# Kernel optimization log

Measured on AMD Instinct MI355X. Metric: run time of the kernel, lower is better.

## Reference

```python
import jax, jax.numpy as jnp
import numpy as np

EPS = 1e-5
TAU = 0.1

def _bn(x, g, b):
    # BatchNorm1d in training mode: batch statistics (biased variance)
    mu = jnp.mean(x, axis=0, keepdims=True)
    var = jnp.var(x, axis=0, keepdims=True)
    return (x - mu) * jax.lax.rsqrt(var + EPS) * g + b

def setup_inputs():
    key = jax.random.key(0)
    ks = jax.random.split(key, 8)
    B, D, H, L, P, C, ND, NP = 32768, 2048, 1024, 384, 192, 10, 2, 2
    s = 0.02
    u = jax.random.uniform(ks[7], (B, NP), minval=1e-6, maxval=1.0 - 1e-6)
    return {
        'x': jax.random.normal(ks[0], (B, D), dtype=jnp.float32),
        'W_pre': jax.random.normal(ks[1], (H, D), dtype=jnp.float32) * s,
        'b_pre': jnp.zeros((H,), jnp.float32),
        'g_pre': jnp.ones((H,), jnp.float32),
        'be_pre': jnp.zeros((H,), jnp.float32),
        'W_disc': jax.random.normal(ks[2], (L, H), dtype=jnp.float32) * s,
        'b_disc': jnp.zeros((L,), jnp.float32),
        'g_disc': jnp.ones((L,), jnp.float32),
        'be_disc': jnp.zeros((L,), jnp.float32),
        'W_dfc': jax.random.normal(ks[3], (ND, L), dtype=jnp.float32) * s,
        'b_dfc': jnp.zeros((ND,), jnp.float32),
        'W_sw': jax.random.normal(ks[4], (NP, L), dtype=jnp.float32) * s,
        'b_sw': jnp.zeros((NP,), jnp.float32),
        'W1': jax.random.normal(ks[5], (NP, P, H), dtype=jnp.float32) * s,
        'b1': jnp.zeros((NP, P), jnp.float32),
        'W2': jax.random.normal(ks[6], (NP, C, P), dtype=jnp.float32) * s,
        'b2': jnp.zeros((NP, C), jnp.float32),
        'gumbel_noise': -jnp.log(-jnp.log(u)),
    }

def reference(x, W_pre, b_pre, g_pre, be_pre, W_disc, b_disc, g_disc, be_disc,
              W_dfc, b_dfc, W_sw, b_sw, W1, b1, W2, b2, gumbel_noise):
    # pre_classifier: Linear + BN + ReLU
    feature = jax.nn.relu(_bn(x @ W_pre.T + b_pre, g_pre, be_pre))
    # GRL is identity in forward
    dp = jax.nn.relu(_bn(feature @ W_disc.T + b_disc, g_disc, be_disc))
    dom = dp @ W_dfc.T + b_dfc                      # [B, num_domains]
    sw = jax.nn.relu(dp @ W_sw.T + b_sw)            # [B, n_partition]
    gum = jax.nn.softmax((sw + gumbel_noise) / TAU, axis=-1)  # soft gumbel-softmax
    idx = jnp.argmax(gum, axis=-1)                  # [B] routing decision
    # compute both (tiny) experts densely, then select per sample (faithful math,
    # avoids per-sample gather of full weight matrices)
    h_all = jax.nn.relu(jnp.einsum('bd,epd->bep', feature, W1) + b1)  # [B,E,P]
    o_all = jnp.einsum('bep,ecp->bec', h_all, W2) + b2                # [B,E,C]
    out = jnp.take_along_axis(o_all, idx[:, None, None], axis=1)[:, 0]  # [B,C]
    # original: sum_p gum[b,p] * stacked (stacked has one entry) == out * sum(gum)
    cop = out * jnp.sum(gum, axis=-1, keepdims=True)
    return cop, dom, idx
```

## Files before the change

### kernel.cpp

```cpp
#include <hip/hip_runtime.h>
#include <math.h>

#define kB 32768
#define kD 2048
#define kH 1024
#define kL 384
#define kP 192
#define kC 10
#define kNP 2
#define kND 2
#define kNCAT 768
#define kTAU 0.1f
#define kEPS 1e-5f
#define NPART 256
#define SCALE 64.0f
#define INV_SC2 (1.0f / 4096.0f)

typedef _Float16 f16x8 __attribute__((ext_vector_type(8)));
typedef _Float16 f16x4 __attribute__((ext_vector_type(4)));
typedef float f32x16 __attribute__((ext_vector_type(16)));

__device__ __forceinline__ void gll16(const unsigned short* g, unsigned short* l)
{
    __builtin_amdgcn_global_load_lds(
        (const __attribute__((address_space(1))) unsigned int*)g,
        (__attribute__((address_space(3))) unsigned int*)l, 16, 0, 0);
}

__device__ __host__ __forceinline__ int key8(int r) { return (r ^ (r >> 3)) & 7; }

__global__ __launch_bounds__(256)
void split_pack(const float* __restrict__ in, unsigned short* __restrict__ out, int K)
{
    const int row = blockIdx.x;
    const int t = threadIdx.x;
    const int s = key8(row);
    const float* ir = in + (size_t)row * K;
    unsigned short* orow = out + (size_t)row * (K * 2);
    for (int k0 = t * 4; k0 < K; k0 += 1024) {
        const float4 v = *(const float4*)&ir[k0];
        const float a0 = v.x * SCALE, a1 = v.y * SCALE, a2 = v.z * SCALE, a3 = v.w * SCALE;
        const _Float16 h0 = (_Float16)a0, h1 = (_Float16)a1, h2 = (_Float16)a2, h3 = (_Float16)a3;
        const _Float16 l0 = (_Float16)(a0 - (float)h0), l1 = (_Float16)(a1 - (float)h1);
        const _Float16 l2 = (_Float16)(a2 - (float)h2), l3 = (_Float16)(a3 - (float)h3);
        const f16x4 hi = {h0, h1, h2, h3};
        const f16x4 lo = {l0, l1, l2, l3};
        const int kb = k0 >> 5, kk = k0 & 31;
        const int c = kk >> 3, off = kk & 7;
        *(f16x4*)&orow[kb * 64 + ((c ^ s) << 3) + off]       = hi;
        *(f16x4*)&orow[kb * 64 + (((c ^ 4) ^ s) << 3) + off] = lo;
    }
}

template<int KDIM, bool BN>
__global__ __launch_bounds__(512, 1)
void gemm_fused(const float* __restrict__ Afp,
                const unsigned short* __restrict__ Bpk,
                const float* __restrict__ bnsc, const float* __restrict__ bnsh,
                float* __restrict__ C, const int N, const int gridX,
                float* __restrict__ psum, float* __restrict__ psumsq, const int statN)
{
    constexpr int NKB = KDIM / 32;
    __shared__ unsigned short lds[4][256 * 64];

    const int t = threadIdx.x;
    const int lane = t & 63;
    const int w = t >> 6;
    const int wr = w >> 2, wc = w & 3;
    const int l31 = lane & 31, kg = lane >> 5;

    const int nwg = gridDim.x;
    const int chunk = nwg >> 3;
    const int bid = blockIdx.x;
    const int logical = (bid & 7) * chunk + (bid >> 3);
    const int bx = logical % gridX, by = logical / gridX;
    const int m0 = by * 256, n0 = bx * 256;

    const int arow = t >> 1;
    const int akh = t & 1;
    const int skey = key8(arow);
    const int c0 = akh * 2, c1 = akh * 2 + 1;
    const float* aSrc = Afp + (size_t)(m0 + arow) * KDIM + akh * 16;

    const size_t bstride = (size_t)NKB * 64;
    const unsigned short* bG[4];
    int bLoff[4];
#pragma unroll
    for (int it = 0; it < 4; ++it) {
        const int Q = (w * 4 + it) * 64 + lane;
        bG[it] = Bpk + (size_t)(n0 + (Q >> 3)) * bstride + (Q & 7) * 8;
        bLoff[it] = (w * 4 + it) * 512;
    }

    int keyA[4], keyB[2];
#pragma unroll
    for (int mi = 0; mi < 4; ++mi)
        keyA[mi] = (l31 & 7) ^ ((mi * 4 + (l31 >> 3)) & 7);
#pragma unroll
    for (int ni = 0; ni < 2; ++ni)
        keyB[ni] = (l31 & 7) ^ ((wc * 8 + ni * 4 + (l31 >> 3)) & 7);

    f32x16 acc[4][2];
#pragma unroll
    for (int mi = 0; mi < 4; ++mi)
#pragma unroll
        for (int ni = 0; ni < 2; ++ni)
#pragma unroll
            for (int r = 0; r < 16; ++r) acc[mi][ni][r] = 0.f;

    float4 av[4], scv[4], shv[4];

    auto stage_issue = [&](int kb, int buf) {
        const int kt = kb * 32;
#pragma unroll
        for (int it = 0; it < 4; ++it)
            gll16(bG[it] + (size_t)kb * 64, &lds[2 + buf][bLoff[it]]);
#pragma unroll
        for (int j = 0; j < 4; ++j)
            av[j] = *(const float4*)&aSrc[kt + j * 4];
        if constexpr (BN) {
#pragma unroll
            for (int j = 0; j < 4; ++j) {
                scv[j] = *(const float4*)&bnsc[kt + akh * 16 + j * 4];
                shv[j] = *(const float4*)&bnsh[kt + akh * 16 + j * 4];
            }
        }
    };

    auto stage_write = [&](int buf) {
        float v[16];
#pragma unroll
        for (int j = 0; j < 4; ++j) {
            float4 a = av[j];
            if constexpr (BN) {
                a.x = fmaxf(fmaf(a.x, scv[j].x, shv[j].x), 0.f);
                a.y = fmaxf(fmaf(a.y, scv[j].y, shv[j].y), 0.f);
                a.z = fmaxf(fmaf(a.z, scv[j].z, shv[j].z), 0.f);
                a.w = fmaxf(fmaf(a.w, scv[j].w, shv[j].w), 0.f);
            } else {
                a.x *= SCALE; a.y *= SCALE; a.z *= SCALE; a.w *= SCALE;
            }
            v[j * 4 + 0] = a.x; v[j * 4 + 1] = a.y;
            v[j * 4 + 2] = a.z; v[j * 4 + 3] = a.w;
        }
        f16x8 hi[2], lo[2];
#pragma unroll
        for (int h = 0; h < 2; ++h)
#pragma unroll
            for (int i = 0; i < 8; ++i) {
                const float x = v[h * 8 + i];
                const _Float16 hh = (_Float16)x;
                hi[h][i] = hh;
                lo[h][i] = (_Float16)(x - (float)hh);
            }
        unsigned short* dst = &lds[buf][arow * 64];
        *(f16x8*)&dst[(c0 ^ skey) * 8]       = hi[0];
        *(f16x8*)&dst[(c1 ^ skey) * 8]       = hi[1];
        *(f16x8*)&dst[((c0 ^ 4) ^ skey) * 8] = lo[0];
        *(f16x8*)&dst[((c1 ^ 4) ^ skey) * 8] = lo[1];
    };

    stage_issue(0, 0);
    stage_write(0);
    asm volatile("s_waitcnt vmcnt(0) lgkmcnt(0)" ::: "memory");
    __builtin_amdgcn_s_barrier();

    for (int kb = 0; kb < NKB; ++kb) {
        const int cur = kb & 1, nxt = cur ^ 1;
        const bool pf = (kb + 1 < NKB);
        if (pf) stage_issue(kb + 1, nxt);

        f16x8 bh[2][2], bl[2][2];
#pragma unroll
        for (int ni = 0; ni < 2; ++ni) {
            const unsigned short* bb = &lds[2 + cur][(wc * 64 + ni * 32 + l31) * 64];
#pragma unroll
            for (int ks = 0; ks < 2; ++ks) {
                const int lg = ks * 2 + kg;
                bh[ni][ks] = *(const f16x8*)&bb[((lg ^ keyB[ni]) << 3)];
                bl[ni][ks] = *(const f16x8*)&bb[(((lg ^ 4) ^ keyB[ni]) << 3)];
            }
        }
#pragma unroll
        for (int mi = 0; mi < 4; ++mi) {
            const unsigned short* ab = &lds[cur][(wr * 128 + mi * 32 + l31) * 64];
            f16x8 ah[2], al[2];
#pragma unroll
            for (int ks = 0; ks < 2; ++ks) {
                const int lg = ks * 2 + kg;
                ah[ks] = *(const f16x8*)&ab[((lg ^ keyA[mi]) << 3)];
                al[ks] = *(const f16x8*)&ab[(((lg ^ 4) ^ keyA[mi]) << 3)];
            }
#pragma unroll
            for (int ni = 0; ni < 2; ++ni)
#pragma unroll
                for (int ks = 0; ks < 2; ++ks) {
                    acc[mi][ni] = __builtin_amdgcn_mfma_f32_32x32x16_f16(ah[ks], bh[ni][ks], acc[mi][ni], 0, 0, 0);
                    acc[mi][ni] = __builtin_amdgcn_mfma_f32_32x32x16_f16(ah[ks], bl[ni][ks], acc[mi][ni], 0, 0, 0);
                    acc[mi][ni] = __builtin_amdgcn_mfma_f32_32x32x16_f16(al[ks], bh[ni][ks], acc[mi][ni], 0, 0, 0);
                }
        }
        if (pf) stage_write(nxt);
        asm volatile("s_waitcnt vmcnt(0) lgkmcnt(0)" ::: "memory");
        __builtin_amdgcn_s_barrier();
    }

#pragma unroll
    for (int mi = 0; mi < 4; ++mi)
#pragma unroll
        for (int ni = 0; ni < 2; ++ni) {
            const int colg = n0 + wc * 64 + ni * 32 + l31;
#pragma unroll
            for (int r = 0; r < 16; ++r) {
                const int row = m0 + wr * 128 + mi * 32 + (r & 3) + 8 * (r >> 2) + 4 * kg;
                C[(size_t)row * N + colg] = acc[mi][ni][r];
            }
        }

#pragma unroll
    for (int ni = 0; ni < 2; ++ni) {
        float s = 0.f, sq = 0.f;
#pragma unroll
        for (int mi = 0; mi < 4; ++mi)
#pragma unroll
            for (int r = 0; r < 16; ++r) {
                const float v = acc[mi][ni][r];
                s += v;
                sq = fmaf(v, v, sq);
            }
        s  += __shfl_xor(s, 32);
        sq += __shfl_xor(sq, 32);
        const int col = n0 + wc * 64 + ni * 32 + l31;
        if (lane < 32 && col < statN) {
            psum[(size_t)(by * 2 + wr) * statN + col]   = s;
            psumsq[(size_t)(by * 2 + wr) * statN + col] = sq;
        }
    }
}

__global__ __launch_bounds__(256)
void colstat_finalize(const float* __restrict__ psum, const float* __restrict__ psumsq,
                      int ncols, const float* __restrict__ g, const float* __restrict__ be,
                      float* __restrict__ scale, float* __restrict__ shift,
                      float inv_sc, float outsc)
{
    const int c = blockIdx.x * 256 + threadIdx.x;
    if (c >= ncols) return;
    float s = 0.f, sq = 0.f;
    for (int i = 0; i < NPART; ++i) {
        s  += psum[(size_t)i * ncols + c];
        sq += psumsq[(size_t)i * ncols + c];
    }
    const float mup = s * (1.f / kB);
    const float var = (sq * (1.f / kB) - mup * mup) * inv_sc * inv_sc;
    const float scl = outsc * g[c] * rsqrtf(var + kEPS) * inv_sc;
    scale[c] = scl;
    shift[c] = fmaf(-mup, scl, outsc * be[c]);
}

__global__ __launch_bounds__(256)
void tail_kernel(const float* __restrict__ Z2,
                 const float* __restrict__ scale2, const float* __restrict__ shift2,
                 const float* __restrict__ W_dfc, const float* __restrict__ b_dfc,
                 const float* __restrict__ W_sw, const float* __restrict__ b_sw,
                 const float* __restrict__ b1, const float* __restrict__ W2,
                 const float* __restrict__ b2, const float* __restrict__ noise,
                 float* __restrict__ out)
{
    __shared__ float sWdfc[kND * kL];
    __shared__ float sWsw[kNP * kL];
    __shared__ float sW2[kNP * kC * kP];
    __shared__ float sb1[kNP * kP];
    __shared__ float sScale[kL];
    __shared__ float sShift[kL];
    const int t = threadIdx.x;
    for (int i = t; i < kND * kL; i += 256) sWdfc[i] = W_dfc[i];
    for (int i = t; i < kNP * kL; i += 256) sWsw[i] = W_sw[i];
    for (int i = t; i < kNP * kC * kP; i += 256) sW2[i] = W2[i];
    for (int i = t; i < kNP * kP; i += 256) sb1[i] = b1[i];
    for (int i = t; i < kL; i += 256) { sScale[i] = scale2[i]; sShift[i] = shift2[i]; }
    __syncthreads();

    const int lane = t & 63;
    const int b = blockIdx.x * 4 + (t >> 6);
    const float* z = Z2 + (size_t)b * kNCAT;

    float d0 = 0.f, d1 = 0.f, s0 = 0.f, s1 = 0.f;
#pragma unroll
    for (int j = 0; j < 6; ++j) {
        const int k = lane + j * 64;
        const float dp = fmaxf(fmaf(z[k], sScale[k], sShift[k]), 0.f);
        d0 = fmaf(dp, sWdfc[k],      d0);
        d1 = fmaf(dp, sWdfc[kL + k], d1);
        s0 = fmaf(dp, sWsw[k],       s0);
        s1 = fmaf(dp, sWsw[kL + k],  s1);
    }
#pragma unroll
    for (int off = 32; off; off >>= 1) {
        d0 += __shfl_xor(d0, off);
        d1 += __shfl_xor(d1, off);
        s0 += __shfl_xor(s0, off);
        s1 += __shfl_xor(s1, off);
    }
    d0 += b_dfc[0];
    d1 += b_dfc[1];

    const float sw0 = fmaxf(s0 + b_sw[0], 0.f);
    const float sw1 = fmaxf(s1 + b_sw[1], 0.f);
    const float l0 = (sw0 + noise[(size_t)b * 2 + 0]) * (1.f / kTAU);
    const float l1 = (sw1 + noise[(size_t)b * 2 + 1]) * (1.f / kTAU);
    const float mx = fmaxf(l0, l1);
    const float e0 = expf(l0 - mx), e1 = expf(l1 - mx);
    const float inv = 1.f / (e0 + e1);
    const float sgum = e0 * inv + e1 * inv;
    const int idx = (l1 > l0) ? 1 : 0;

    const float* zh = z + kL + idx * kP;
    const float h0 = fmaxf(fmaf(zh[lane],       INV_SC2, sb1[idx * kP + lane]),       0.f);
    const float h1 = fmaxf(fmaf(zh[lane + 64],  INV_SC2, sb1[idx * kP + lane + 64]),  0.f);
    const float h2 = fmaxf(fmaf(zh[lane + 128], INV_SC2, sb1[idx * kP + lane + 128]), 0.f);

    float* cop  = out;
    float* dom  = out + (size_t)kB * kC;
    float* idxo = dom + (size_t)kB * kND;

#pragma unroll
    for (int c = 0; c < kC; ++c) {
        const float* wv = &sW2[(idx * kC + c) * kP];
        float oc = h0 * wv[lane] + h1 * wv[lane + 64] + h2 * wv[lane + 128];
#pragma unroll
        for (int off = 32; off; off >>= 1) oc += __shfl_xor(oc, off);
        if (lane == c) cop[(size_t)b * kC + c] = (oc + b2[idx * kC + c]) * sgum;
    }
    if (lane == 0) {
        dom[(size_t)b * 2 + 0] = d0;
        dom[(size_t)b * 2 + 1] = d1;
        idxo[b] = (float)idx;
    }
}

extern "C" void kernel_launch(void* const* d_in, const int* in_sizes, int n_in,
                              void* d_out, int out_size, void* d_ws, size_t ws_size,
                              hipStream_t stream)
{
    const float* x       = (const float*)d_in[0];
    const float* W_pre   = (const float*)d_in[1];
    const float* g_pre   = (const float*)d_in[3];
    const float* be_pre  = (const float*)d_in[4];
    const float* W_disc  = (const float*)d_in[5];
    const float* g_disc  = (const float*)d_in[7];
    const float* be_disc = (const float*)d_in[8];
    const float* W_dfc   = (const float*)d_in[9];
    const float* b_dfc   = (const float*)d_in[10];
    const float* W_sw    = (const float*)d_in[11];
    const float* b_sw    = (const float*)d_in[12];
    const float* W1      = (const float*)d_in[13];
    const float* b1      = (const float*)d_in[14];
    const float* W2      = (const float*)d_in[15];
    const float* b2      = (const float*)d_in[16];
    const float* noise   = (const float*)d_in[17];

    char* wsb = (char*)d_ws;
    unsigned short* Wps = (unsigned short*)wsb;
    unsigned short* Ws2 = (unsigned short*)(wsb + (size_t)1024 * 4096 * 2);
    float* Z1 = (float*)(wsb + (size_t)1024 * 4096 * 2 + (size_t)768 * 2048 * 2);
    float* Z2 = Z1 + (size_t)kB * kH;
    float* psum1  = Z2 + (size_t)kB * kNCAT;
    float* psq1   = psum1 + (size_t)NPART * kH;
    float* psum2  = psq1 + (size_t)NPART * kH;
    float* psq2   = psum2 + (size_t)NPART * kL;
    float* scale1 = psq2 + (size_t)NPART * kL;
    float* shift1 = scale1 + kH;
    float* scale2 = shift1 + kH;
    float* shift2 = scale2 + kL;
    float* out    = (float*)d_out;

    split_pack<<<dim3(kH), 256, 0, stream>>>(W_pre, Wps, kD);
    split_pack<<<dim3(kL), 256, 0, stream>>>(W_disc, Ws2, kH);
    split_pack<<<dim3(kNP * kP), 256, 0, stream>>>(W1, Ws2 + (size_t)kL * (2 * kH), kH);
    gemm_fused<kD, false><<<dim3(4 * 128), 512, 0, stream>>>(
        x, Wps, nullptr, nullptr, Z1, kH, 4, psum1, psq1, kH);
    colstat_finalize<<<dim3(kH / 256), 256, 0, stream>>>(psum1, psq1, kH, g_pre, be_pre,
                                                         scale1, shift1, INV_SC2, SCALE);
    gemm_fused<kH, true><<<dim3(3 * 128), 512, 0, stream>>>(
        Z1, Ws2, scale1, shift1, Z2, kNCAT, 3, psum2, psq2, kL);
    colstat_finalize<<<dim3((kL + 255) / 256), 256, 0, stream>>>(psum2, psq2, kL, g_disc, be_disc,
                                                                 scale2, shift2, INV_SC2, 1.0f);
    tail_kernel<<<dim3(kB / 4), 256, 0, stream>>>(Z2, scale2, shift2, W_dfc, b_dfc,
                                                  W_sw, b_sw, b1, W2, b2, noise, out);
}
```

Baseline: 691.1 us.

## Pre-split activations to fp16 hi/lo and stream both GEMM operands via LDS DMA

Adds separate passes that convert x, and later the BN+ReLU-applied Z1, into swizzled fp16 hi/lo packed buffers. Both GEMMs then load A and B tiles with global_load_lds DMA into 128x128 tiles at 256 threads with occupancy 3, replacing the 256x256 double-buffered kernel that converted A in registers. The aim is to take conversion ALU work and register pressure out of the GEMM inner loop and to rely on more resident workgroups for latency hiding. In exchange it adds extra global traffic: the packed x buffer is twice the size of x in fp32 and has to be written and then read back, and the main loop is single-buffered with two barriers per k-step.

```diff
diff --git a/kernel.cpp b/kernel.cpp
--- a/kernel.cpp
+++ b/kernel.cpp
@@ -12,12 +12,11 @@
 #define kNCAT 768
 #define kTAU 0.1f
 #define kEPS 1e-5f
-#define NPART 256
+#define NPART 512
 #define SCALE 64.0f
 #define INV_SC2 (1.0f / 4096.0f)
 
 typedef _Float16 f16x8 __attribute__((ext_vector_type(8)));
-typedef _Float16 f16x4 __attribute__((ext_vector_type(4)));
 typedef float f32x16 __attribute__((ext_vector_type(16)));
 
 __device__ __forceinline__ void gll16(const unsigned short* g, unsigned short* l)
@@ -27,192 +26,165 @@
         (__attribute__((address_space(3))) unsigned int*)l, 16, 0, 0);
 }
 
-__device__ __host__ __forceinline__ int key8(int r) { return (r ^ (r >> 3)) & 7; }
+__device__ __host__ __forceinline__ int wkey(int r)
+{
+    return (r & 1) | ((r & 2) << 1) | ((r & 4) >> 1);
+}
 
 __global__ __launch_bounds__(256)
-void split_pack(const float* __restrict__ in, unsigned short* __restrict__ out, int K)
-{
-    const int row = blockIdx.x;
-    const int t = threadIdx.x;
-    const int s = key8(row);
-    const float* ir = in + (size_t)row * K;
-    unsigned short* orow = out + (size_t)row * (K * 2);
-    for (int k0 = t * 4; k0 < K; k0 += 1024) {
-        const float4 v = *(const float4*)&ir[k0];
-        const float a0 = v.x * SCALE, a1 = v.y * SCALE, a2 = v.z * SCALE, a3 = v.w * SCALE;
-        const _Float16 h0 = (_Float16)a0, h1 = (_Float16)a1, h2 = (_Float16)a2, h3 = (_Float16)a3;
-        const _Float16 l0 = (_Float16)(a0 - (float)h0), l1 = (_Float16)(a1 - (float)h1);
-        const _Float16 l2 = (_Float16)(a2 - (float)h2), l3 = (_Float16)(a3 - (float)h3);
-        const f16x4 hi = {h0, h1, h2, h3};
-        const f16x4 lo = {l0, l1, l2, l3};
-        const int kb = k0 >> 5, kk = k0 & 31;
-        const int c = kk >> 3, off = kk & 7;
-        *(f16x4*)&orow[kb * 64 + ((c ^ s) << 3) + off]       = hi;
-        *(f16x4*)&orow[kb * 64 + (((c ^ 4) ^ s) << 3) + off] = lo;
-    }
-}
-
-template<int KDIM, bool BN>
-__global__ __launch_bounds__(512, 1)
-void gemm_fused(const float* __restrict__ Afp,
-                const unsigned short* __restrict__ Bpk,
-                const float* __restrict__ bnsc, const float* __restrict__ bnsh,
-                float* __restrict__ C, const int N, const int gridX,
-                float* __restrict__ psum, float* __restrict__ psumsq, const int statN)
+void split_pack(const float* __restrict__ in, unsigned short* __restrict__ out,
+                int lognkb, int total)
+{
+    const int gid = blockIdx.x * 256 + threadIdx.x;
+    if (gid >= total) return;
+    const int nkb = 1 << lognkb;
+    const int row = gid >> lognkb;
+    const int kb  = gid & (nkb - 1);
+    const float* src = in + ((size_t)row << (lognkb + 5)) + kb * 32;
+    unsigned short* dst = out + ((size_t)row << (lognkb + 6)) + kb * 64;
+    const int s = wkey(row & 7);
+#pragma unroll
+    for (int h = 0; h < 4; ++h) {
+        const float4 a = *(const float4*)&src[h * 8];
+        const float4 b = *(const float4*)&src[h * 8 + 4];
+        const float v[8] = {a.x, a.y, a.z, a.w, b.x, b.y, b.z, b.w};
+        f16x8 hi, lo;
+#pragma unroll
+        for (int i = 0; i < 8; ++i) {
+            const float x = v[i] * SCALE;
+            const _Float16 hh = (_Float16)x;
+            hi[i] = hh;
+            lo[i] = (_Float16)(x - (float)hh);
+        }
+        *(f16x8*)&dst[((h ^ s) << 3)]       = hi;
+        *(f16x8*)&dst[(((h ^ 4) ^ s) << 3)] = lo;
+    }
+}
+
+__global__ __launch_bounds__(256)
+void split_bn(const float* __restrict__ Z, const float* __restrict__ scl,
+              const float* __restrict__ shf, unsigned short* __restrict__ out)
+{
+    const int gid = blockIdx.x * 256 + threadIdx.x;
+    const int row = gid >> 5, kb = gid & 31;
+    const float* src = Z + (size_t)row * kH + kb * 32;
+    unsigned short* dst = out + (size_t)row * 2048 + kb * 64;
+    const int s = wkey(row & 7);
+#pragma unroll
+    for (int h = 0; h < 4; ++h) {
+        const float4 a  = *(const float4*)&src[h * 8];
+        const float4 b  = *(const float4*)&src[h * 8 + 4];
+        const float4 c0 = *(const float4*)&scl[kb * 32 + h * 8];
+        const float4 c1 = *(const float4*)&scl[kb * 32 + h * 8 + 4];
+        const float4 d0 = *(const float4*)&shf[kb * 32 + h * 8];
+        const float4 d1 = *(const float4*)&shf[kb * 32 + h * 8 + 4];
+        const float v[8] = {
+            fmaxf(fmaf(a.x, c0.x, d0.x), 0.f), fmaxf(fmaf(a.y, c0.y, d0.y), 0.f),
+            fmaxf(fmaf(a.z, c0.z, d0.z), 0.f), fmaxf(fmaf(a.w, c0.w, d0.w), 0.f),
+            fmaxf(fmaf(b.x, c1.x, d1.x), 0.f), fmaxf(fmaf(b.y, c1.y, d1.y), 0.f),
+            fmaxf(fmaf(b.z, c1.z, d1.z), 0.f), fmaxf(fmaf(b.w, c1.w, d1.w), 0.f)};
+        f16x8 hi, lo;
+#pragma unroll
+        for (int i = 0; i < 8; ++i) {
+            const _Float16 hh = (_Float16)v[i];
+            hi[i] = hh;
+            lo[i] = (_Float16)(v[i] - (float)hh);
+        }
+        *(f16x8*)&dst[((h ^ s) << 3)]       = hi;
+        *(f16x8*)&dst[(((h ^ 4) ^ s) << 3)] = lo;
+    }
+}
+
+template<int KDIM>
+__global__ __launch_bounds__(256, 3)
+void gemm_dma(const unsigned short* __restrict__ Apk,
+              const unsigned short* __restrict__ Bpk,
+              float* __restrict__ C, const int N, const int gridX,
+              float* __restrict__ psum, float* __restrict__ psumsq, const int statN)
 {
     constexpr int NKB = KDIM / 32;
-    __shared__ unsigned short lds[4][256 * 64];
+    __shared__ __align__(16) unsigned short As_[128 * 64];
+    __shared__ __align__(16) unsigned short Bs_[128 * 64];
 
     const int t = threadIdx.x;
     const int lane = t & 63;
     const int w = t >> 6;
-    const int wr = w >> 2, wc = w & 3;
+    const int wr = w >> 1, wc = w & 1;
     const int l31 = lane & 31, kg = lane >> 5;
+    const int key = wkey(l31 & 7);
 
     const int nwg = gridDim.x;
     const int chunk = nwg >> 3;
     const int bid = blockIdx.x;
     const int logical = (bid & 7) * chunk + (bid >> 3);
     const int bx = logical % gridX, by = logical / gridX;
-    const int m0 = by * 256, n0 = bx * 256;
-
-    const int arow = t >> 1;
-    const int akh = t & 1;
-    const int skey = key8(arow);
-    const int c0 = akh * 2, c1 = akh * 2 + 1;
-    const float* aSrc = Afp + (size_t)(m0 + arow) * KDIM + akh * 16;
-
-    const size_t bstride = (size_t)NKB * 64;
+    const int m0 = by * 128, n0 = bx * 128;
+
+    const size_t stride = (size_t)NKB * 64;
+    const unsigned short* aG[4];
     const unsigned short* bG[4];
-    int bLoff[4];
+    int loff[4];
 #pragma unroll
     for (int it = 0; it < 4; ++it) {
         const int Q = (w * 4 + it) * 64 + lane;
-        bG[it] = Bpk + (size_t)(n0 + (Q >> 3)) * bstride + (Q & 7) * 8;
-        bLoff[it] = (w * 4 + it) * 512;
-    }
-
-    int keyA[4], keyB[2];
-#pragma unroll
-    for (int mi = 0; mi < 4; ++mi)
-        keyA[mi] = (l31 & 7) ^ ((mi * 4 + (l31 >> 3)) & 7);
-#pragma unroll
-    for (int ni = 0; ni < 2; ++ni)
-        keyB[ni] = (l31 & 7) ^ ((wc * 8 + ni * 4 + (l31 >> 3)) & 7);
-
-    f32x16 acc[4][2];
-#pragma unroll
-    for (int mi = 0; mi < 4; ++mi)
+        const int row = Q >> 3, c = Q & 7;
+        aG[it] = Apk + (size_t)(m0 + row) * stride + c * 8;
+        bG[it] = Bpk + (size_t)(n0 + row) * stride + c * 8;
+        loff[it] = (w * 4 + it) * 512;
+    }
+
+    f32x16 acc[2][2];
+#pragma unroll
+    for (int mi = 0; mi < 2; ++mi)
 #pragma unroll
         for (int ni = 0; ni < 2; ++ni)
 #pragma unroll
             for (int r = 0; r < 16; ++r) acc[mi][ni][r] = 0.f;
 
-    float4 av[4], scv[4], shv[4];
-
-    auto stage_issue = [&](int kb, int buf) {
-        const int kt = kb * 32;
-#pragma unroll
-        for (int it = 0; it < 4; ++it)
-            gll16(bG[it] + (size_t)kb * 64, &lds[2 + buf][bLoff[it]]);
-#pragma unroll
-        for (int j = 0; j < 4; ++j)
-            av[j] = *(const float4*)&aSrc[kt + j * 4];
-        if constexpr (BN) {
-#pragma unroll
-            for (int j = 0; j < 4; ++j) {
-                scv[j] = *(const float4*)&bnsc[kt + akh * 16 + j * 4];
-                shv[j] = *(const float4*)&bnsh[kt + akh * 16 + j * 4];
+    for (int kb = 0; kb < NKB; ++kb) {
+        const size_t ko = (size_t)kb * 64;
+#pragma unroll
+        for (int it = 0; it < 4; ++it) {
+            gll16(aG[it] + ko, &As_[loff[it]]);
+            gll16(bG[it] + ko, &Bs_[loff[it]]);
+        }
+        __syncthreads();
+
+#pragma unroll
+        for (int ks = 0; ks < 2; ++ks) {
+            const int ch = (ks * 2 + kg) ^ key;
+            const int cl = ch ^ 4;
+            f16x8 bh[2], bl[2];
+#pragma unroll
+            for (int ni = 0; ni < 2; ++ni) {
+                const unsigned short* bb = &Bs_[(wc * 64 + ni * 32 + l31) * 64];
+                bh[ni] = *(const f16x8*)&bb[ch * 8];
+                bl[ni] = *(const f16x8*)&bb[cl * 8];
             }
-        }
-    };
-
-    auto stage_write = [&](int buf) {
-        float v[16];
-#pragma unroll
-        for (int j = 0; j < 4; ++j) {
-            float4 a = av[j];
-            if constexpr (BN) {
-                a.x = fmaxf(fmaf(a.x, scv[j].x, shv[j].x), 0.f);
-                a.y = fmaxf(fmaf(a.y, scv[j].y, shv[j].y), 0.f);
-                a.z = fmaxf(fmaf(a.z, scv[j].z, shv[j].z), 0.f);
-                a.w = fmaxf(fmaf(a.w, scv[j].w, shv[j].w), 0.f);
-            } else {
-                a.x *= SCALE; a.y *= SCALE; a.z *= SCALE; a.w *= SCALE;
+#pragma unroll
+            for (int mi = 0; mi < 2; ++mi) {
+                const unsigned short* ab = &As_[(wr * 64 + mi * 32 + l31) * 64];
+                const f16x8 ah = *(const f16x8*)&ab[ch * 8];
+                const f16x8 al = *(const f16x8*)&ab[cl * 8];
+#pragma unroll
+                for (int ni = 0; ni < 2; ++ni) {
+                    acc[mi][ni] = __builtin_amdgcn_mfma_f32_32x32x16_f16(ah, bh[ni], acc[mi][ni], 0, 0, 0);
+                    acc[mi][ni] = __builtin_amdgcn_mfma_f32_32x32x16_f16(ah, bl[ni], acc[mi][ni], 0, 0, 0);
+                    acc[mi][ni] = __builtin_amdgcn_mfma_f32_32x32x16_f16(al, bh[ni], acc[mi][ni], 0, 0, 0);
+                }
             }
-            v[j * 4 + 0] = a.x; v[j * 4 + 1] = a.y;
-            v[j * 4 + 2] = a.z; v[j * 4 + 3] = a.w;
-        }
-        f16x8 hi[2], lo[2];
-#pragma unroll
-        for (int h = 0; h < 2; ++h)
-#pragma unroll
-            for (int i = 0; i < 8; ++i) {
-                const float x = v[h * 8 + i];
-                const _Float16 hh = (_Float16)x;
-                hi[h][i] = hh;
-                lo[h][i] = (_Float16)(x - (float)hh);
-            }
-        unsigned short* dst = &lds[buf][arow * 64];
-        *(f16x8*)&dst[(c0 ^ skey) * 8]       = hi[0];
-        *(f16x8*)&dst[(c1 ^ skey) * 8]       = hi[1];
-        *(f16x8*)&dst[((c0 ^ 4) ^ skey) * 8] = lo[0];
-        *(f16x8*)&dst[((c1 ^ 4) ^ skey) * 8] = lo[1];
-    };
-
-    stage_issue(0, 0);
-    stage_write(0);
-    asm volatile("s_waitcnt vmcnt(0) lgkmcnt(0)" ::: "memory");
-    __builtin_amdgcn_s_barrier();
-
-    for (int kb = 0; kb < NKB; ++kb) {
-        const int cur = kb & 1, nxt = cur ^ 1;
-        const bool pf = (kb + 1 < NKB);
-        if (pf) stage_issue(kb + 1, nxt);
-
-        f16x8 bh[2][2], bl[2][2];
-#pragma unroll
-        for (int ni = 0; ni < 2; ++ni) {
-            const unsigned short* bb = &lds[2 + cur][(wc * 64 + ni * 32 + l31) * 64];
-#pragma unroll
-            for (int ks = 0; ks < 2; ++ks) {
-                const int lg = ks * 2 + kg;
-                bh[ni][ks] = *(const f16x8*)&bb[((lg ^ keyB[ni]) << 3)];
-                bl[ni][ks] = *(const f16x8*)&bb[(((lg ^ 4) ^ keyB[ni]) << 3)];
-            }
-        }
-#pragma unroll
-        for (int mi = 0; mi < 4; ++mi) {
-            const unsigned short* ab = &lds[cur][(wr * 128 + mi * 32 + l31) * 64];
-            f16x8 ah[2], al[2];
-#pragma unroll
-            for (int ks = 0; ks < 2; ++ks) {
-                const int lg = ks * 2 + kg;
-                ah[ks] = *(const f16x8*)&ab[((lg ^ keyA[mi]) << 3)];
-                al[ks] = *(const f16x8*)&ab[(((lg ^ 4) ^ keyA[mi]) << 3)];
-            }
-#pragma unroll
-            for (int ni = 0; ni < 2; ++ni)
-#pragma unroll
-                for (int ks = 0; ks < 2; ++ks) {
-                    acc[mi][ni] = __builtin_amdgcn_mfma_f32_32x32x16_f16(ah[ks], bh[ni][ks], acc[mi][ni], 0, 0, 0);
-                    acc[mi][ni] = __builtin_amdgcn_mfma_f32_32x32x16_f16(ah[ks], bl[ni][ks], acc[mi][ni], 0, 0, 0);
-                    acc[mi][ni] = __builtin_amdgcn_mfma_f32_32x32x16_f16(al[ks], bh[ni][ks], acc[mi][ni], 0, 0, 0);
-                }
-        }
-        if (pf) stage_write(nxt);
-        asm volatile("s_waitcnt vmcnt(0) lgkmcnt(0)" ::: "memory");
-        __builtin_amdgcn_s_barrier();
-    }
-
-#pragma unroll
-    for (int mi = 0; mi < 4; ++mi)
+        }
+        __syncthreads();
+    }
+
+#pragma unroll
+    for (int mi = 0; mi < 2; ++mi)
 #pragma unroll
         for (int ni = 0; ni < 2; ++ni) {
             const int colg = n0 + wc * 64 + ni * 32 + l31;
 #pragma unroll
             for (int r = 0; r < 16; ++r) {
-                const int row = m0 + wr * 128 + mi * 32 + (r & 3) + 8 * (r >> 2) + 4 * kg;
+                const int row = m0 + wr * 64 + mi * 32 + (r & 3) + 8 * (r >> 2) + 4 * kg;
                 C[(size_t)row * N + colg] = acc[mi][ni][r];
             }
         }
@@ -221,7 +193,7 @@
     for (int ni = 0; ni < 2; ++ni) {
         float s = 0.f, sq = 0.f;
 #pragma unroll
-        for (int mi = 0; mi < 4; ++mi)
+        for (int mi = 0; mi < 2; ++mi)
 #pragma unroll
             for (int r = 0; r < 16; ++r) {
                 const float v = acc[mi][ni][r];
@@ -361,11 +333,16 @@
     const float* noise   = (const float*)d_in[17];
 
     char* wsb = (char*)d_ws;
-    unsigned short* Wps = (unsigned short*)wsb;
-    unsigned short* Ws2 = (unsigned short*)(wsb + (size_t)1024 * 4096 * 2);
-    float* Z1 = (float*)(wsb + (size_t)1024 * 4096 * 2 + (size_t)768 * 2048 * 2);
-    float* Z2 = Z1 + (size_t)kB * kH;
-    float* psum1  = Z2 + (size_t)kB * kNCAT;
+    const size_t xs_bytes  = (size_t)kB * (2 * kD) * 2;
+    const size_t wps_bytes = (size_t)kH * (2 * kD) * 2;
+    const size_t ws2_bytes = (size_t)kNCAT * (2 * kH) * 2;
+    unsigned short* xs  = (unsigned short*)wsb;
+    unsigned short* Fs  = xs;
+    float* Z2 = (float*)(wsb + (size_t)kB * (2 * kH) * 2);
+    unsigned short* Wps = (unsigned short*)(wsb + xs_bytes);
+    unsigned short* Ws2 = (unsigned short*)(wsb + xs_bytes + wps_bytes);
+    float* Z1 = (float*)(wsb + xs_bytes + wps_bytes + ws2_bytes);
+    float* psum1  = Z1 + (size_t)kB * kH;
     float* psq1   = psum1 + (size_t)NPART * kH;
     float* psum2  = psq1 + (size_t)NPART * kH;
     float* psq2   = psum2 + (size_t)NPART * kL;
@@ -375,15 +352,18 @@
     float* shift2 = scale2 + kL;
     float* out    = (float*)d_out;
 
-    split_pack<<<dim3(kH), 256, 0, stream>>>(W_pre, Wps, kD);
-    split_pack<<<dim3(kL), 256, 0, stream>>>(W_disc, Ws2, kH);
-    split_pack<<<dim3(kNP * kP), 256, 0, stream>>>(W1, Ws2 + (size_t)kL * (2 * kH), kH);
-    gemm_fused<kD, false><<<dim3(4 * 128), 512, 0, stream>>>(
-        x, Wps, nullptr, nullptr, Z1, kH, 4, psum1, psq1, kH);
+    split_pack<<<dim3(kB * 64 / 256), 256, 0, stream>>>(x, xs, 6, kB * 64);
+    split_pack<<<dim3(kH * 64 / 256), 256, 0, stream>>>(W_pre, Wps, 6, kH * 64);
+    split_pack<<<dim3(kL * 32 / 256), 256, 0, stream>>>(W_disc, Ws2, 5, kL * 32);
+    split_pack<<<dim3(kNP * kP * 32 / 256), 256, 0, stream>>>(
+        W1, Ws2 + (size_t)kL * (2 * kH), 5, kNP * kP * 32);
+    gemm_dma<kD><<<dim3(8 * 256), 256, 0, stream>>>(
+        xs, Wps, Z1, kH, 8, psum1, psq1, kH);
     colstat_finalize<<<dim3(kH / 256), 256, 0, stream>>>(psum1, psq1, kH, g_pre, be_pre,
                                                          scale1, shift1, INV_SC2, SCALE);
-    gemm_fused<kH, true><<<dim3(3 * 128), 512, 0, stream>>>(
-        Z1, Ws2, scale1, shift1, Z2, kNCAT, 3, psum2, psq2, kL);
+    split_bn<<<dim3(kB * 32 / 256), 256, 0, stream>>>(Z1, scale1, shift1, Fs);
+    gemm_dma<kH><<<dim3(6 * 256), 256, 0, stream>>>(
+        Fs, Ws2, Z2, kNCAT, 6, psum2, psq2, kL);
     colstat_finalize<<<dim3((kL + 255) / 256), 256, 0, stream>>>(psum2, psq2, kL, g_disc, be_disc,
                                                                  scale2, shift2, INV_SC2, 1.0f);
     tail_kernel<<<dim3(kB / 4), 256, 0, stream>>>(Z2, scale2, shift2, W_dfc, b_dfc,
```

Result: slower. 927.1 us (+34.2%).
